# Kernel tuning notes

Measured on AMD Instinct MI355X. Metric: run time of the kernel, lower is better.

Reference implementation:

```python
import jax, jax.numpy as jnp
import numpy as np

N_NODES = 200000
N_EDGES = 240000
HIDDEN = 128
N_TYPES = 6


def setup_inputs() -> dict:
    key = jax.random.key(0)
    k1, k2, k3, k4, k5 = jax.random.split(key, 5)
    state_embedding = jax.random.normal(k1, (N_NODES, HIDDEN), dtype=jnp.float32)
    # row 0: edge type in [1, N_TYPES]; row 1: source node; row 2: target node
    etype = jax.random.randint(k2, (N_EDGES,), 1, N_TYPES + 1, dtype=jnp.int32)
    src = jax.random.randint(k3, (N_EDGES,), 0, N_NODES, dtype=jnp.int32)
    tgt = jax.random.randint(k4, (N_EDGES,), 0, N_NODES, dtype=jnp.int32)
    typed_edges = jnp.stack([etype, src, tgt], axis=0)  # [3, E]
    # stacked per-edge-type Linear(2H, H, bias=False) weights, applied as x @ W[t]
    W = jax.random.normal(k5, (N_TYPES, 2 * HIDDEN, HIDDEN), dtype=jnp.float32) / np.sqrt(2 * HIDDEN)
    return {"state_embedding": state_embedding, "typed_edges": typed_edges, "W": W}


def reference(state_embedding, typed_edges, W):
    etype, src, tgt = typed_edges[0], typed_edges[1], typed_edges[2]
    # gather source/target node states and concat -> [E, 2H]
    x = jnp.concatenate([state_embedding[src], state_embedding[tgt]], axis=1)
    n_types = W.shape[0]
    msgs = jnp.zeros((x.shape[0], W.shape[2]), dtype=x.dtype)
    # fixed small loop over edge types; masking replaces the dynamic boolean
    # filtering of the torch code (edges with type t use only W[t-1])
    for t in range(n_types):
        mask = (etype == t + 1)[:, None]
        msgs = msgs + jnp.where(mask, x @ W[t], jnp.zeros((), x.dtype))
    # scatter-add messages into target node slots, dim_size = num nodes
    return jax.ops.segment_sum(msgs, tgt, num_segments=state_embedding.shape[0])
```

## Files before the change

kernel.cpp:

```cpp
#include <hip/hip_runtime.h>

#define NTYPES 6
#define HID 128
#define E_TILE 64
#define TPB 4

typedef short short8 __attribute__((ext_vector_type(8)));
typedef float f32x4 __attribute__((ext_vector_type(4)));

static __device__ __forceinline__ ushort f2bf(float f) {
    union { float f; unsigned u; } v; v.f = f;
    unsigned r = v.u + 0x7FFFu + ((v.u >> 16) & 1u);
    return (ushort)(r >> 16);
}


__global__ void k_prep(int4* __restrict__ zp, int n4,
                       const float* __restrict__ Sf, ushort* __restrict__ Sb, int total,
                       const float* __restrict__ W, ushort* __restrict__ Wt,
                       int zb, int sb) {
    int b = blockIdx.x;
    if (b < zb) {
        int i = b * 256 + threadIdx.x;
        if (i < n4) zp[i] = make_int4(0, 0, 0, 0);
    } else if (b < zb + sb) {
        int g = ((b - zb) * 256 + threadIdx.x) * 8;
        if (g < total) {
            float4 a = *(const float4*)(Sf + g);
            float4 c = *(const float4*)(Sf + g + 4);
            ushort t[8] = { f2bf(a.x), f2bf(a.y), f2bf(a.z), f2bf(a.w),
                            f2bf(c.x), f2bf(c.y), f2bf(c.z), f2bf(c.w) };
            *(short8*)(Sb + g) = *(short8*)t;
        }
    } else {
        int t = (b - zb - sb) * 256 + threadIdx.x;
        int n  = t & 127;
        int k8 = (t >> 7) & 31;
        int ty = t >> 12;
        if (ty >= NTYPES) return;
        const float* wp = W + ((size_t)ty * 256 + (size_t)k8 * 8) * HID + n;
        ushort tmp[8];
        #pragma unroll
        for (int j = 0; j < 8; ++j) tmp[j] = f2bf(wp[(size_t)j * HID]);
        *(short8*)(Wt + ((size_t)ty * HID + n) * 256 + k8 * 8) = *(short8*)tmp;
    }
}

template <int RANK>
__global__ void k_bin(const int* __restrict__ etype, const int* __restrict__ tgt, int E, int CAP,
                      int* __restrict__ hdr, int* __restrict__ ncnt,
                      int* __restrict__ arr, int* __restrict__ sortedT) {
    __shared__ int lcnt[NTYPES];
    __shared__ int lbase[NTYPES];
    if (threadIdx.x < NTYPES) lcnt[threadIdx.x] = 0;
    __syncthreads();
    int i = blockIdx.x * 256 + threadIdx.x;
    int t = 0, lr = 0;
    bool valid = (i < E);
    if (valid) {
        t = etype[i] - 1;
        lr = atomicAdd(&lcnt[t], 1);
        if (RANK) arr[i] = atomicAdd(&ncnt[tgt[i]], 1);
    }
    __syncthreads();
    if (threadIdx.x < NTYPES) {
        int c = lcnt[threadIdx.x];
        lbase[threadIdx.x] = c ? atomicAdd(&hdr[16 + threadIdx.x], c) : 0;
    }
    __syncthreads();
    if (valid) {
        int pos = lbase[t] + lr;
        if (pos < CAP) sortedT[t * CAP + pos] = i;
    }
}

__global__ void k_scan1(const int* __restrict__ ncnt, int* __restrict__ noff,
                        int* __restrict__ bsum, int N) {
    __shared__ int s[256];
    const int b = blockIdx.x, t = threadIdx.x;
    const int base = b * 1024 + t * 4;
    int v[4];
    #pragma unroll
    for (int i = 0; i < 4; ++i) v[i] = (base + i < N) ? ncnt[base + i] : 0;
    int tsum = v[0] + v[1] + v[2] + v[3];
    s[t] = tsum;
    __syncthreads();
    for (int off = 1; off < 256; off <<= 1) {
        int x = (t >= off) ? s[t - off] : 0;
        __syncthreads();
        s[t] += x;
        __syncthreads();
    }
    if (t == 255) bsum[b] = s[255];
    int run = s[t] - tsum;
    #pragma unroll
    for (int i = 0; i < 4; ++i)
        if (base + i < N) { noff[base + i] = run; run += v[i]; }
}

__global__ void k_scan2(int* __restrict__ bsum, int nb) {
    __shared__ int s[256];
    const int t = threadIdx.x;
    int v = (t < nb) ? bsum[t] : 0;
    s[t] = v;
    __syncthreads();
    for (int off = 1; off < 256; off <<= 1) {
        int x = (t >= off) ? s[t - off] : 0;
        __syncthreads();
        s[t] += x;
        __syncthreads();
    }
    if (t < nb) bsum[t] = s[t] - v;
}

__global__ void k_wconv(const float* __restrict__ W, ushort* __restrict__ Wt) {
    int t = blockIdx.x * blockDim.x + threadIdx.x;
    int n  = t & 127;
    int k8 = (t >> 7) & 31;
    int ty = t >> 12;
    if (ty >= NTYPES) return;
    const float* wp = W + ((size_t)ty * 256 + (size_t)k8 * 8) * HID + n;
    ushort tmp[8];
    #pragma unroll
    for (int j = 0; j < 8; ++j) tmp[j] = f2bf(wp[(size_t)j * HID]);
    *(short8*)(Wt + ((size_t)ty * HID + n) * 256 + k8 * 8) = *(short8*)tmp;
}

__global__ void k_zero32(int* __restrict__ p) {
    if (threadIdx.x < 32) p[threadIdx.x] = 0;
}

template <int MODE>
__launch_bounds__(256, 4)
__global__ void k_gemm(const ushort* __restrict__ Sb, const float* __restrict__ Sf,
                       const int* __restrict__ src, const int* __restrict__ tgt,
                       const ushort* __restrict__ Wt, const int* __restrict__ hdr,
                       const int* __restrict__ sortedT, int CAP,
                       const int* __restrict__ noff, const int* __restrict__ bsum,
                       const int* __restrict__ arr,
                       ushort* __restrict__ msgs, float* __restrict__ out) {
    __shared__ __align__(16) ushort Xs[E_TILE][264];
    __shared__ int sN[TPB][E_TILE];
    __shared__ int tN[TPB][E_TILE];
    __shared__ int dstR[TPB][E_TILE];

    int g = blockIdx.x;
    int ty, t0 = 0, ntl = 0, cnt_t = 0;
    for (ty = 0; ty < NTYPES; ++ty) {
        int c = hdr[16 + ty];
        if (c > CAP) c = CAP;
        int nt = (c + E_TILE - 1) >> 6;
        int ng = (nt + TPB - 1) / TPB;
        if (g < ng) {
            t0 = g * TPB;
            ntl = nt - t0; if (ntl > TPB) ntl = TPB;
            cnt_t = c;
            break;
        }
        g -= ng;
    }
    if (ty == NTYPES) return;

    const int tid = threadIdx.x;
    const int w  = tid >> 6;
    const int l  = tid & 63;
    const int lr = l & 15;
    const int lg = l >> 4;

    {
        const int tt = tid >> 6, s = l;
        if (tt < ntl) {
            int gidx = (t0 + tt) * E_TILE + s;
            int sn = 0, tn = 0, dr = 0;
            if (gidx < cnt_t) {
                int e = sortedT[ty * CAP + gidx];
                sn = src[e]; tn = tgt[e];
                if (MODE == 2) dr = noff[tn] + bsum[tn >> 10] + arr[e];
            }
            sN[tt][s] = sn; tN[tt][s] = tn; dstR[tt][s] = dr;
        }
    }

    short8 wreg[16];
    {
        const ushort* wb = Wt + ((size_t)ty * HID + w * 32 + lr) * 256 + 8 * lg;
        #pragma unroll
        for (int kk = 0; kk < 8; ++kk) {
            wreg[2 * kk]     = *(const short8*)(wb + kk * 32);
            wreg[2 * kk + 1] = *(const short8*)(wb + 16 * 256 + kk * 32);
        }
    }
    __syncthreads();

    for (int tt = 0; tt < ntl; ++tt) {
        int cnt = cnt_t - (t0 + tt) * E_TILE;
        if (cnt > E_TILE) cnt = E_TILE;

        {
            const int e = tid >> 2, q = tid & 3;
            ushort* dp = &Xs[e][q * 64];
            if (e < cnt) {
                const int node = (q & 2) ? tN[tt][e] : sN[tt][e];
                if (MODE == 2) {
                    const ushort* rp = Sb + (size_t)node * HID + (q & 1) * 64;
                    short8 v[8];
                    #pragma unroll
                    for (int i = 0; i < 8; ++i) v[i] = *(const short8*)(rp + i * 8);
                    #pragma unroll
                    for (int i = 0; i < 8; ++i) *(short8*)(dp + i * 8) = v[i];
                } else {
                    const float* rp = Sf + (size_t)node * HID + (q & 1) * 64;
                    #pragma unroll
                    for (int i = 0; i < 8; ++i) {
                        float4 a = *(const float4*)(rp + i * 8);
                        float4 b = *(const float4*)(rp + i * 8 + 4);
                        ushort tmp[8] = { f2bf(a.x), f2bf(a.y), f2bf(a.z), f2bf(a.w),
                                          f2bf(b.x), f2bf(b.y), f2bf(b.z), f2bf(b.w) };
                        *(short8*)(dp + i * 8) = *(short8*)tmp;
                    }
                }
            } else {
                short8 z = (short8){0, 0, 0, 0, 0, 0, 0, 0};
                #pragma unroll
                for (int i = 0; i < 8; ++i) *(short8*)(dp + i * 8) = z;
            }
        }
        __syncthreads();

        f32x4 acc[4][2];
        #pragma unroll
        for (int mf = 0; mf < 4; ++mf)
            #pragma unroll
            for (int nf = 0; nf < 2; ++nf)
                acc[mf][nf] = (f32x4){0.f, 0.f, 0.f, 0.f};

        const ushort* xb = &Xs[lr][8 * lg];
        #pragma unroll
        for (int kk = 0; kk < 8; ++kk) {
            const int k0 = kk * 32;
            #pragma unroll
            for (int mf = 0; mf < 4; ++mf) {
                short8 a = *(const short8*)(xb + mf * 16 * 264 + k0);
                acc[mf][0] = __builtin_amdgcn_mfma_f32_16x16x32_bf16(a, wreg[2 * kk],     acc[mf][0], 0, 0, 0);
                acc[mf][1] = __builtin_amdgcn_mfma_f32_16x16x32_bf16(a, wreg[2 * kk + 1], acc[mf][1], 0, 0, 0);
            }
        }
        __syncthreads();

        float (*Os)[132] = (float (*)[132])&Xs[0][0];
        #pragma unroll
        for (int mf = 0; mf < 4; ++mf)
            #pragma unroll
            for (int nf = 0; nf < 2; ++nf)
                #pragma unroll
                for (int r = 0; r < 4; ++r)
                    Os[mf * 16 + lg * 4 + r][w * 32 + nf * 16 + lr] = acc[mf][nf][r];
        __syncthreads();

        if (MODE == 2) {
            const int r8 = tid >> 4, cg = tid & 15;
            #pragma unroll
            for (int rr = 0; rr < 4; ++rr) {
                int row = rr * 16 + r8;
                if (row < cnt) {
                    float4 a = *(const float4*)&Os[row][cg * 8];
                    float4 b = *(const float4*)&Os[row][cg * 8 + 4];
                    ushort tmp[8] = { f2bf(a.x), f2bf(a.y), f2bf(a.z), f2bf(a.w),
                                      f2bf(b.x), f2bf(b.y), f2bf(b.z), f2bf(b.w) };
                    *(short8*)(msgs + (size_t)dstR[tt][row] * HID + cg * 8) = *(short8*)tmp;
                }
            }
        } else {
            const int rA = tid >> 7;
            const int c  = tid & (HID - 1);
            for (int it = 0; it < E_TILE / 2; ++it) {
                int ee = it * 2 + rA;
                if (ee < cnt) atomicAdd(&out[(size_t)tN[tt][ee] * HID + c], Os[ee][c]);
            }
        }
        __syncthreads();
    }
}

__launch_bounds__(256)
__global__ void k_scatter(const ushort* __restrict__ msgs, const int* __restrict__ noff,
                          const int* __restrict__ bsum, float* __restrict__ out,
                          int N, int Etot) {
    int node = blockIdx.x * 4 + (threadIdx.x >> 6);
    if (node >= N) return;
    int cp = threadIdx.x & 63;
    int s = noff[node] + bsum[node >> 10];
    int e = (node + 1 < N) ? (noff[node + 1] + bsum[(node + 1) >> 10]) : Etot;
    float a0 = 0.f, a1 = 0.f;
    for (int r = s; r < e; ++r) {
        unsigned u = *(const unsigned*)(msgs + (size_t)r * HID + cp * 2);
        union { unsigned u; float f; } lo, hi;
        lo.u = u << 16; hi.u = u & 0xFFFF0000u;
        a0 += lo.f; a1 += hi.f;
    }
    *(float2*)(out + (size_t)node * HID + cp * 2) = make_float2(a0, a1);
}

extern "C" void kernel_launch(void* const* d_in, const int* in_sizes, int n_in,
                              void* d_out, int out_size, void* d_ws, size_t ws_size,
                              hipStream_t stream) {
    const float* Sf    = (const float*)d_in[0];
    const int*   edges = (const int*)d_in[1];
    const float* W     = (const float*)d_in[2];
    float* out = (float*)d_out;

    const int E = in_sizes[1] / 3;
    const int N = in_sizes[0] / HID;
    const int* etype = edges;
    const int* src   = edges + E;
    const int* tgt   = edges + 2 * E;
    int* ws = (int*)d_ws;

    const int CAP = E / 5 + 4096;

    int* ncnt    = ws + 32;
    int* noff    = ncnt + N;
    int* bsum    = noff + N + 1;
    int* arr     = bsum + 256;
    int* sortedT = arr + E;
    size_t intsEnd = (size_t)(32 + N + (N + 1) + 256 + (size_t)E + 6 * (size_t)CAP) * sizeof(int);
    size_t wtOff   = (intsEnd + 255) & ~(size_t)255;
    size_t sbOff   = ((wtOff + (size_t)NTYPES * HID * 256 * 2) + 255) & ~(size_t)255;
    size_t msgsOff = ((sbOff + (size_t)N * HID * 2) + 255) & ~(size_t)255;
    size_t need2   = msgsOff + (size_t)E * HID * 2;

    const int nb1 = (N + 1023) / 1024;
    const int nblocks = (E + E_TILE * TPB - 1) / (E_TILE * TPB) + 2 * NTYPES;
    const int eb = (E + 255) / 256;
    ushort* Wt = (ushort*)((char*)d_ws + wtOff);

    if (ws_size >= need2 && nb1 <= 256) {
        ushort* Sb   = (ushort*)((char*)d_ws + sbOff);
        ushort* msgs = (ushort*)((char*)d_ws + msgsOff);
        const int total = N * HID;
        const int n4 = (32 + N + 3) / 4;
        const int zb = (n4 + 255) / 256;
        const int sb = (total / 8 + 255) / 256;
        const int wb = (NTYPES * HID * 32 + 255) / 256;

        k_prep<<<zb + sb + wb, 256, 0, stream>>>((int4*)ws, n4, Sf, Sb, total, W, Wt, zb, sb);
        k_bin<1><<<eb, 256, 0, stream>>>(etype, tgt, E, CAP, ws, ncnt, arr, sortedT);
        k_scan1<<<nb1, 256, 0, stream>>>(ncnt, noff, bsum, N);
        k_scan2<<<1, 256, 0, stream>>>(bsum, nb1);
        k_gemm<2><<<nblocks, 256, 0, stream>>>(Sb, Sf, src, tgt, Wt, ws, sortedT, CAP,
                                               noff, bsum, arr, msgs, out);
        k_scatter<<<(N + 3) / 4, 256, 0, stream>>>(msgs, noff, bsum, out, N, E);
    } else {
        int* sortedT0 = ws + 32;
        size_t wt0Off = (((size_t)(32 + 6 * (size_t)CAP) * sizeof(int)) + 255) & ~(size_t)255;
        ushort* Wt0 = (ushort*)((char*)d_ws + wt0Off);

        k_zero32<<<1, 64, 0, stream>>>(ws);
        hipMemsetAsync(d_out, 0, (size_t)out_size * sizeof(float), stream);
        k_bin<0><<<eb, 256, 0, stream>>>(etype, tgt, E, CAP, ws, nullptr, nullptr, sortedT0);
        k_wconv<<<(NTYPES * HID * 32) / 256, 256, 0, stream>>>(W, Wt0);
        k_gemm<0><<<nblocks, 256, 0, stream>>>(nullptr, Sf, src, tgt, Wt0, ws, sortedT0, CAP,
                                               nullptr, nullptr, nullptr, nullptr, out);
    }
}
```

Measured before the change: 138.0 us.

## Bin edges by type and target bucket, pack indices, bypass scatter for degree-one nodes

Edges are now binned into regions keyed by edge type and a coarse target-node bucket, each storing a packed (src, tgt|rank) pair. This removes the indirect src/tgt/arr loads in the GEMM and improves locality of output writes. GEMM blocks are remapped across the 8 XCDs. Nodes with exactly one incoming edge get their fp32 message written straight to the output, and the scatter kernel skips them. The cost is a fixed per-region capacity: a region that exceeds it would silently drop edges.

```diff
diff --git a/kernel.cpp b/kernel.cpp
--- a/kernel.cpp
+++ b/kernel.cpp
@@ -4,6 +4,10 @@
 #define HID 128
 #define E_TILE 64
 #define TPB 4
+#define BBUCK 64
+#define NREG (NTYPES * BBUCK)
+#define TNBITS 19
+#define TNMASK ((1 << TNBITS) - 1)
 
 typedef short short8 __attribute__((ext_vector_type(8)));
 typedef float f32x4 __attribute__((ext_vector_type(4)));
@@ -47,30 +51,36 @@
 }
 
 template <int RANK>
-__global__ void k_bin(const int* __restrict__ etype, const int* __restrict__ tgt, int E, int CAP,
-                      int* __restrict__ hdr, int* __restrict__ ncnt,
-                      int* __restrict__ arr, int* __restrict__ sortedT) {
-    __shared__ int lcnt[NTYPES];
-    __shared__ int lbase[NTYPES];
-    if (threadIdx.x < NTYPES) lcnt[threadIdx.x] = 0;
+__global__ void k_bin(const int* __restrict__ etype, const int* __restrict__ src,
+                      const int* __restrict__ tgt, int E, int CAP, int shift,
+                      int* __restrict__ rcur, int* __restrict__ ncnt,
+                      int2* __restrict__ sortedT2) {
+    __shared__ int lcnt[NREG];
+    __shared__ int lbase[NREG];
+    for (int r = threadIdx.x; r < NREG; r += 256) lcnt[r] = 0;
     __syncthreads();
     int i = blockIdx.x * 256 + threadIdx.x;
-    int t = 0, lr = 0;
     bool valid = (i < E);
+    int sn = 0, pk = 0, reg = 0, lrk = 0;
     if (valid) {
-        t = etype[i] - 1;
-        lr = atomicAdd(&lcnt[t], 1);
-        if (RANK) arr[i] = atomicAdd(&ncnt[tgt[i]], 1);
-    }
-    __syncthreads();
-    if (threadIdx.x < NTYPES) {
-        int c = lcnt[threadIdx.x];
-        lbase[threadIdx.x] = c ? atomicAdd(&hdr[16 + threadIdx.x], c) : 0;
+        int t  = etype[i] - 1;
+        int tn = tgt[i];
+        sn = src[i];
+        int a = 0;
+        if (RANK) a = atomicAdd(&ncnt[tn], 1);
+        pk  = tn | (a << TNBITS);
+        reg = t * BBUCK + (tn >> shift);
+        lrk = atomicAdd(&lcnt[reg], 1);
+    }
+    __syncthreads();
+    for (int r = threadIdx.x; r < NREG; r += 256) {
+        int c = lcnt[r];
+        lbase[r] = c ? atomicAdd(&rcur[r], c) : 0;
     }
     __syncthreads();
     if (valid) {
-        int pos = lbase[t] + lr;
-        if (pos < CAP) sortedT[t * CAP + pos] = i;
+        int pos = lbase[reg] + lrk;
+        if (pos < CAP) sortedT2[(size_t)reg * CAP + pos] = make_int2(sn, pk);
     }
 }
 
@@ -113,53 +123,32 @@
     if (t < nb) bsum[t] = s[t] - v;
 }
 
-__global__ void k_wconv(const float* __restrict__ W, ushort* __restrict__ Wt) {
-    int t = blockIdx.x * blockDim.x + threadIdx.x;
-    int n  = t & 127;
-    int k8 = (t >> 7) & 31;
-    int ty = t >> 12;
-    if (ty >= NTYPES) return;
-    const float* wp = W + ((size_t)ty * 256 + (size_t)k8 * 8) * HID + n;
-    ushort tmp[8];
-    #pragma unroll
-    for (int j = 0; j < 8; ++j) tmp[j] = f2bf(wp[(size_t)j * HID]);
-    *(short8*)(Wt + ((size_t)ty * HID + n) * 256 + k8 * 8) = *(short8*)tmp;
-}
-
-__global__ void k_zero32(int* __restrict__ p) {
-    if (threadIdx.x < 32) p[threadIdx.x] = 0;
-}
-
 template <int MODE>
 __launch_bounds__(256, 4)
 __global__ void k_gemm(const ushort* __restrict__ Sb, const float* __restrict__ Sf,
-                       const int* __restrict__ src, const int* __restrict__ tgt,
-                       const ushort* __restrict__ Wt, const int* __restrict__ hdr,
-                       const int* __restrict__ sortedT, int CAP,
-                       const int* __restrict__ noff, const int* __restrict__ bsum,
-                       const int* __restrict__ arr,
+                       const ushort* __restrict__ Wt, const int* __restrict__ rcur,
+                       const int2* __restrict__ sortedT2, int CAP, int G,
+                       const int* __restrict__ ncnt, const int* __restrict__ noff,
+                       const int* __restrict__ bsum,
                        ushort* __restrict__ msgs, float* __restrict__ out) {
     __shared__ __align__(16) ushort Xs[E_TILE][264];
     __shared__ int sN[TPB][E_TILE];
     __shared__ int tN[TPB][E_TILE];
     __shared__ int dstR[TPB][E_TILE];
 
-    int g = blockIdx.x;
-    int ty, t0 = 0, ntl = 0, cnt_t = 0;
-    for (ty = 0; ty < NTYPES; ++ty) {
-        int c = hdr[16 + ty];
-        if (c > CAP) c = CAP;
-        int nt = (c + E_TILE - 1) >> 6;
-        int ng = (nt + TPB - 1) / TPB;
-        if (g < ng) {
-            t0 = g * TPB;
-            ntl = nt - t0; if (ntl > TPB) ntl = TPB;
-            cnt_t = c;
-            break;
-        }
-        g -= ng;
-    }
-    if (ty == NTYPES) return;
+    int nwg = gridDim.x;
+    int qq = nwg >> 3, rm = nwg & 7;
+    int xcd = blockIdx.x & 7, io = blockIdx.x >> 3;
+    int bid = (xcd < rm) ? xcd * (qq + 1) + io : rm * (qq + 1) + (xcd - rm) * qq + io;
+
+    int reg = bid / G, g = bid - reg * G;
+    int ty  = reg >> 6;
+    int cnt_r = rcur[reg]; if (cnt_r > CAP) cnt_r = CAP;
+    int nt  = (cnt_r + E_TILE - 1) >> 6;
+    int ntl = nt - g * TPB;
+    if (ntl <= 0) return;
+    if (ntl > TPB) ntl = TPB;
+    const int base = g * TPB * E_TILE;
 
     const int tid = threadIdx.x;
     const int w  = tid >> 6;
@@ -170,12 +159,17 @@
     {
         const int tt = tid >> 6, s = l;
         if (tt < ntl) {
-            int gidx = (t0 + tt) * E_TILE + s;
+            int gp = base + tt * E_TILE + s;
             int sn = 0, tn = 0, dr = 0;
-            if (gidx < cnt_t) {
-                int e = sortedT[ty * CAP + gidx];
-                sn = src[e]; tn = tgt[e];
-                if (MODE == 2) dr = noff[tn] + bsum[tn >> 10] + arr[e];
+            if (gp < cnt_r) {
+                int2 v = sortedT2[(size_t)reg * CAP + gp];
+                sn = v.x;
+                tn = v.y & TNMASK;
+                if (MODE == 2) {
+                    int a = ((unsigned)v.y) >> TNBITS;
+                    dr = (ncnt[tn] == 1) ? -(tn + 1)
+                                         : (noff[tn] + bsum[tn >> 10] + a);
+                }
             }
             sN[tt][s] = sn; tN[tt][s] = tn; dstR[tt][s] = dr;
         }
@@ -193,7 +187,7 @@
     __syncthreads();
 
     for (int tt = 0; tt < ntl; ++tt) {
-        int cnt = cnt_t - (t0 + tt) * E_TILE;
+        int cnt = cnt_r - (base + tt * E_TILE);
         if (cnt > E_TILE) cnt = E_TILE;
 
         {
@@ -258,16 +252,23 @@
         __syncthreads();
 
         if (MODE == 2) {
-            const int r8 = tid >> 4, cg = tid & 15;
+            const int r8e = tid >> 4, cg = tid & 15;
             #pragma unroll
             for (int rr = 0; rr < 4; ++rr) {
-                int row = rr * 16 + r8;
+                int row = rr * 16 + r8e;
                 if (row < cnt) {
+                    int dr = dstR[tt][row];
                     float4 a = *(const float4*)&Os[row][cg * 8];
                     float4 b = *(const float4*)&Os[row][cg * 8 + 4];
-                    ushort tmp[8] = { f2bf(a.x), f2bf(a.y), f2bf(a.z), f2bf(a.w),
-                                      f2bf(b.x), f2bf(b.y), f2bf(b.z), f2bf(b.w) };
-                    *(short8*)(msgs + (size_t)dstR[tt][row] * HID + cg * 8) = *(short8*)tmp;
+                    if (dr >= 0) {
+                        ushort tmp[8] = { f2bf(a.x), f2bf(a.y), f2bf(a.z), f2bf(a.w),
+                                          f2bf(b.x), f2bf(b.y), f2bf(b.z), f2bf(b.w) };
+                        *(short8*)(msgs + (size_t)dr * HID + cg * 8) = *(short8*)tmp;
+                    } else {
+                        float* op = out + (size_t)(-dr - 1) * HID + cg * 8;
+                        *(float4*)op = a;
+                        *(float4*)(op + 4) = b;
+                    }
                 }
             }
         } else {
@@ -291,6 +292,7 @@
     int cp = threadIdx.x & 63;
     int s = noff[node] + bsum[node >> 10];
     int e = (node + 1 < N) ? (noff[node + 1] + bsum[(node + 1) >> 10]) : Etot;
+    if (e - s == 1) return;
     float a0 = 0.f, a1 = 0.f;
     for (int r = s; r < e; ++r) {
         unsigned u = *(const unsigned*)(msgs + (size_t)r * HID + cp * 2);
@@ -316,50 +318,53 @@
     const int* tgt   = edges + 2 * E;
     int* ws = (int*)d_ws;
 
-    const int CAP = E / 5 + 4096;
-
-    int* ncnt    = ws + 32;
-    int* noff    = ncnt + N;
-    int* bsum    = noff + N + 1;
-    int* arr     = bsum + 256;
-    int* sortedT = arr + E;
-    size_t intsEnd = (size_t)(32 + N + (N + 1) + 256 + (size_t)E + 6 * (size_t)CAP) * sizeof(int);
-    size_t wtOff   = (intsEnd + 255) & ~(size_t)255;
+    int shift = 0;
+    while (((N - 1) >> shift) >= BBUCK) shift++;
+    const int nbuck = ((N - 1) >> shift) + 1;
+    int mean = E / (NTYPES * nbuck); if (mean < 1) mean = 1;
+    int CAP = ((mean + mean / 2 + 255) / 256) * 256; if (CAP < 256) CAP = 256;
+    const int G = CAP >> 8;
+
+    int* rcur = ws;
+    int* ncnt = ws + NREG;
+    int* noff = ncnt + N;
+    int* bsum = noff + N + 1;
+    size_t intsEnd = (size_t)(NREG + N + (N + 1) + 256) * sizeof(int);
+    size_t st2Off  = (intsEnd + 255) & ~(size_t)255;
+    size_t wtOff   = ((st2Off + (size_t)NREG * CAP * sizeof(int2)) + 255) & ~(size_t)255;
     size_t sbOff   = ((wtOff + (size_t)NTYPES * HID * 256 * 2) + 255) & ~(size_t)255;
     size_t msgsOff = ((sbOff + (size_t)N * HID * 2) + 255) & ~(size_t)255;
     size_t need2   = msgsOff + (size_t)E * HID * 2;
 
     const int nb1 = (N + 1023) / 1024;
-    const int nblocks = (E + E_TILE * TPB - 1) / (E_TILE * TPB) + 2 * NTYPES;
-    const int eb = (E + 255) / 256;
+    const int eb  = (E + 255) / 256;
+    const int ngemm = NREG * G;
     ushort* Wt = (ushort*)((char*)d_ws + wtOff);
-
-    if (ws_size >= need2 && nb1 <= 256) {
+    int2* sortedT2 = (int2*)((char*)d_ws + st2Off);
+
+    if (ws_size >= need2 && nb1 <= 256 && N < (1 << TNBITS)) {
         ushort* Sb   = (ushort*)((char*)d_ws + sbOff);
         ushort* msgs = (ushort*)((char*)d_ws + msgsOff);
         const int total = N * HID;
-        const int n4 = (32 + N + 3) / 4;
+        const int n4 = (NREG + N + 3) / 4;
         const int zb = (n4 + 255) / 256;
         const int sb = (total / 8 + 255) / 256;
         const int wb = (NTYPES * HID * 32 + 255) / 256;
 
         k_prep<<<zb + sb + wb, 256, 0, stream>>>((int4*)ws, n4, Sf, Sb, total, W, Wt, zb, sb);
-        k_bin<1><<<eb, 256, 0, stream>>>(etype, tgt, E, CAP, ws, ncnt, arr, sortedT);
+        k_bin<1><<<eb, 256, 0, stream>>>(etype, src, tgt, E, CAP, shift, rcur, ncnt, sortedT2);
         k_scan1<<<nb1, 256, 0, stream>>>(ncnt, noff, bsum, N);
         k_scan2<<<1, 256, 0, stream>>>(bsum, nb1);
-        k_gemm<2><<<nblocks, 256, 0, stream>>>(Sb, Sf, src, tgt, Wt, ws, sortedT, CAP,
-                                               noff, bsum, arr, msgs, out);
+        k_gemm<2><<<ngemm, 256, 0, stream>>>(Sb, Sf, Wt, rcur, sortedT2, CAP, G,
+                                             ncnt, noff, bsum, msgs, out);
         k_scatter<<<(N + 3) / 4, 256, 0, stream>>>(msgs, noff, bsum, out, N, E);
     } else {
-        int* sortedT0 = ws + 32;
-        size_t wt0Off = (((size_t)(32 + 6 * (size_t)CAP) * sizeof(int)) + 255) & ~(size_t)255;
-        ushort* Wt0 = (ushort*)((char*)d_ws + wt0Off);
-
-        k_zero32<<<1, 64, 0, stream>>>(ws);
+        const int n4 = (NREG + 3) / 4;
+        k_prep<<<1 + (NTYPES * HID * 32 + 255) / 256, 256, 0, stream>>>(
+            (int4*)ws, n4, nullptr, nullptr, 0, W, Wt, 1, 0);
         hipMemsetAsync(d_out, 0, (size_t)out_size * sizeof(float), stream);
-        k_bin<0><<<eb, 256, 0, stream>>>(etype, tgt, E, CAP, ws, nullptr, nullptr, sortedT0);
-        k_wconv<<<(NTYPES * HID * 32) / 256, 256, 0, stream>>>(W, Wt0);
-        k_gemm<0><<<nblocks, 256, 0, stream>>>(nullptr, Sf, src, tgt, Wt0, ws, sortedT0, CAP,
-                                               nullptr, nullptr, nullptr, nullptr, out);
-    }
-}
+        k_bin<0><<<eb, 256, 0, stream>>>(etype, src, tgt, E, CAP, shift, rcur, nullptr, sortedT2);
+        k_gemm<0><<<ngemm, 256, 0, stream>>>(nullptr, Sf, Wt, rcur, sortedT2, CAP, G,
+                                             nullptr, nullptr, nullptr, nullptr, out);
+    }
+}
```

Result: slower. 153.8 us (+11.5%).
